# Performance work log

Hardware: AMD Instinct MI355X
Metric: run time of the kernel (lower is better)

Reference implementation:

```python
import jax, jax.numpy as jnp
import numpy as np

USER_NUM = 100000
ITEM_NUM = 50000
D = 64
E = 3200000
B = 16384


def setup_inputs() -> dict:
    key = jax.random.key(0)
    ks = jax.random.split(key, 12)
    user = jax.random.randint(ks[0], (B,), 0, USER_NUM)
    item_i = jax.random.randint(ks[1], (B,), 0, ITEM_NUM)
    item_j = jax.random.randint(ks[2], (B,), 0, ITEM_NUM)
    edge_u = jax.random.randint(ks[3], (E,), 0, USER_NUM)
    edge_i = jax.random.randint(ks[4], (E,), 0, ITEM_NUM)
    edge_val = jax.random.uniform(ks[5], (E,), dtype=jnp.float32)
    # nn.init.normal_(std=0.01)
    user_emb = 0.01 * jax.random.normal(ks[6], (USER_NUM, D), dtype=jnp.float32)
    item_emb = 0.01 * jax.random.normal(ks[7], (ITEM_NUM, D), dtype=jnp.float32)
    old_U_emb = 0.01 * jax.random.normal(ks[8], (USER_NUM, D), dtype=jnp.float32)
    old_I_emb = 0.01 * jax.random.normal(ks[9], (ITEM_NUM, D), dtype=jnp.float32)
    n_U = jax.random.uniform(ks[10], (USER_NUM,), dtype=jnp.float32)
    n_U = n_U / jnp.linalg.norm(n_U)  # pre_self normalizes by L2 norm
    n_I = jax.random.uniform(ks[11], (ITEM_NUM,), dtype=jnp.float32)
    n_I = n_I / jnp.linalg.norm(n_I)
    return {"user": user, "item_i": item_i, "item_j": item_j,
            "edge_u": edge_u, "edge_i": edge_i, "edge_val": edge_val,
            "user_emb": user_emb, "item_emb": item_emb,
            "old_U_emb": old_U_emb, "old_I_emb": old_I_emb,
            "n_U": n_U, "n_I": n_I}


def _spmm(seg_ids, gather_ids, vals, x, num_segments):
    # one hop of sparse adjacency @ dense embeddings: gather -> scale -> scatter-add
    msg = vals[:, None] * x[gather_ids]          # [E, D]
    return jax.ops.segment_sum(msg, seg_ids, num_segments=num_segments)


def reference(user, item_i, item_j, edge_u, edge_i, edge_val,
              user_emb, item_emb, old_U_emb, old_I_emb, n_U, n_I):
    # 3-hop LightGCN-style propagation over bipartite graph
    g1u = _spmm(edge_u, edge_i, edge_val, item_emb, USER_NUM)
    g1i = _spmm(edge_i, edge_u, edge_val, user_emb, ITEM_NUM)
    g2u = _spmm(edge_u, edge_i, edge_val, g1i, USER_NUM)
    g2i = _spmm(edge_i, edge_u, edge_val, g1u, ITEM_NUM)
    g3u = _spmm(edge_u, edge_i, edge_val, g2i, USER_NUM)
    g3i = _spmm(edge_i, edge_u, edge_val, g2u, ITEM_NUM)
    gcn_u = user_emb + 0.5 * g1u + (1.0 / 3.0) * g2u + 0.25 * g3u
    gcn_i = item_emb + 0.5 * g1i + (1.0 / 3.0) * g2i + 0.25 * g3i

    # BPR loss
    u = gcn_u[user]
    ii = gcn_i[item_i]
    ij = gcn_i[item_j]
    pred_i = jnp.sum(u * ii, axis=-1)
    pred_j = jnp.sum(u * ij, axis=-1)
    bpr = -jnp.mean(jax.nn.log_sigmoid(pred_i - pred_j))
    reg = 1e-4 * jnp.mean(jnp.sum(u ** 2 + ii ** 2 + ij ** 2, axis=-1))
    loss_bpr = bpr + reg

    # self-distillation loss (loss_self)
    Ud = jnp.linalg.norm(old_U_emb - gcn_u, axis=1)  # [USER_NUM]
    Id = jnp.linalg.norm(old_I_emb - gcn_i, axis=1)  # [ITEM_NUM]
    loss_self = jnp.dot(Ud, n_U) / USER_NUM + jnp.dot(Id, n_I) / ITEM_NUM

    return jnp.stack([loss_bpr, 100.0 * loss_self,
                      jnp.float32(1.0), jnp.float32(1.0)])
```

## Files before the change

kernel.cpp:

```cpp
#include <hip/hip_runtime.h>

#define USER_NUM 100000
#define ITEM_NUM 50000
#define DD 64
#define NEDGE 3200000
#define NB 16384
#define NSLOT 256

#define ATILE 8192
#define NTILE ((NEDGE + ATILE - 1) / ATILE)
#define USH 9
#define ISH 8
#define UBK ((USER_NUM + (1 << USH) - 1) >> USH)
#define IBK ((ITEM_NUM + (1 << ISH) - 1) >> ISH)
#define NBK (UBK + IBK)
#define CPAD 16
#define HIST_GRID 784

#define FP8_SCALE 64.0f

typedef float v2f __attribute__((ext_vector_type(2)));

__device__ __forceinline__ float waveReduceSum(float x) {
#pragma unroll
    for (int off = 32; off > 0; off >>= 1)
        x += __shfl_down(x, off, 64);
    return x;
}

__device__ __forceinline__ unsigned roundbf(unsigned y) {
    return (y + 0x7fffu + ((y >> 16) & 1u)) >> 16;
}

__device__ __forceinline__ void dec8(const uint2 b, float* f) {
    v2f f0 = __builtin_amdgcn_cvt_pk_f32_fp8(b.x, false);
    v2f f1 = __builtin_amdgcn_cvt_pk_f32_fp8(b.x, true);
    v2f f2 = __builtin_amdgcn_cvt_pk_f32_fp8(b.y, false);
    v2f f3 = __builtin_amdgcn_cvt_pk_f32_fp8(b.y, true);
    f[0] = f0.x; f[1] = f0.y; f[2] = f1.x; f[3] = f1.y;
    f[4] = f2.x; f[5] = f2.y; f[6] = f3.x; f[7] = f3.y;
}
__device__ __forceinline__ void fma8p(const uint2 b, const float v, v2f* a) {
    v2f f0 = __builtin_amdgcn_cvt_pk_f32_fp8(b.x, false);
    v2f f1 = __builtin_amdgcn_cvt_pk_f32_fp8(b.x, true);
    v2f f2 = __builtin_amdgcn_cvt_pk_f32_fp8(b.y, false);
    v2f f3 = __builtin_amdgcn_cvt_pk_f32_fp8(b.y, true);
    const v2f vv = {v, v};
    a[0] += vv * f0;
    a[1] += vv * f1;
    a[2] += vv * f2;
    a[3] += vv * f3;
}
__device__ __forceinline__ uint2 pack_fp8x8(const float* a) {
    int lo = 0, hi = 0;
    lo = __builtin_amdgcn_cvt_pk_fp8_f32(a[0], a[1], lo, false);
    lo = __builtin_amdgcn_cvt_pk_fp8_f32(a[2], a[3], lo, true);
    hi = __builtin_amdgcn_cvt_pk_fp8_f32(a[4], a[5], hi, false);
    hi = __builtin_amdgcn_cvt_pk_fp8_f32(a[6], a[7], hi, true);
    return make_uint2((unsigned)lo, (unsigned)hi);
}

__global__ void __launch_bounds__(256) cvt8_kernel(
    const float4* __restrict__ src, uint2* __restrict__ dst, int n8) {
    int t = blockIdx.x * blockDim.x + threadIdx.x;
    if (t < n8) {
        float4 a = src[2 * t], b = src[2 * t + 1];
        float f[8] = {a.x * FP8_SCALE, a.y * FP8_SCALE, a.z * FP8_SCALE, a.w * FP8_SCALE,
                      b.x * FP8_SCALE, b.y * FP8_SCALE, b.z * FP8_SCALE, b.w * FP8_SCALE};
        dst[t] = pack_fp8x8(f);
    }
}


__global__ void __launch_bounds__(256) coarse_hist(
    const int4* __restrict__ eu4, const int4* __restrict__ ei4,
    int* __restrict__ coarseCnt) {
    __shared__ int lc[NBK];
    const int t = threadIdx.x;
    for (int j = t; j < NBK; j += 256) lc[j] = 0;
    __syncthreads();
    for (int k = blockIdx.x * 256 + t; k < NEDGE / 4; k += HIST_GRID * 256) {
        int4 u = eu4[k];
        int4 i = ei4[k];
        atomicAdd(&lc[u.x >> USH], 1); atomicAdd(&lc[u.y >> USH], 1);
        atomicAdd(&lc[u.z >> USH], 1); atomicAdd(&lc[u.w >> USH], 1);
        atomicAdd(&lc[UBK + (i.x >> ISH)], 1); atomicAdd(&lc[UBK + (i.y >> ISH)], 1);
        atomicAdd(&lc[UBK + (i.z >> ISH)], 1); atomicAdd(&lc[UBK + (i.w >> ISH)], 1);
    }
    __syncthreads();
    for (int j = t; j < NBK; j += 256)
        if (lc[j]) atomicAdd(&coarseCnt[j * CPAD], lc[j]);
}

__global__ void __launch_bounds__(512) coarse_scan(
    const int* __restrict__ cnt, int* __restrict__ base, int* __restrict__ cur) {
    __shared__ int a[512];
    const int t = threadIdx.x;
    int v = (t < UBK) ? cnt[t * CPAD] : 0;
    a[t] = v;
    __syncthreads();
    for (int off = 1; off < 512; off <<= 1) {
        int x = (t >= off) ? a[t - off] : 0;
        __syncthreads();
        a[t] += x;
        __syncthreads();
    }
    if (t < UBK) { base[t] = a[t] - v; cur[t * CPAD] = a[t] - v; }
    __syncthreads();
    v = (t < IBK) ? cnt[(UBK + t) * CPAD] : 0;
    a[t] = v;
    __syncthreads();
    for (int off = 1; off < 512; off <<= 1) {
        int x = (t >= off) ? a[t - off] : 0;
        __syncthreads();
        a[t] += x;
        __syncthreads();
    }
    if (t < IBK) { base[UBK + t] = a[t] - v; cur[(UBK + t) * CPAD] = a[t] - v; }
}

__global__ void __launch_bounds__(256, 2) binA(
    const int* __restrict__ eu, const int* __restrict__ ei,
    const float* __restrict__ ev,
    int* __restrict__ ccur,
    int2* __restrict__ stU, int2* __restrict__ stI) {
    __shared__ int2 pay[ATILE];
    __shared__ unsigned char sbid[ATILE];
    __shared__ int hist[256];
    __shared__ int pscan[256];
    __shared__ int cursor[256];
    __shared__ int delta[256];

    const int t = threadIdx.x;
    const int dirI = blockIdx.y;
    const int tb = blockIdx.x * ATILE;
    const int n = min(ATILE, NEDGE - tb);
    const int* key = dirI ? ei : eu;
    const int SH = dirI ? ISH : USH;

    hist[t] = 0;
    __syncthreads();
    for (int k = t; k < n; k += 256)
        atomicAdd(&hist[key[tb + k] >> SH], 1);
    __syncthreads();
    pscan[t] = hist[t];
    __syncthreads();
    for (int off = 1; off < 256; off <<= 1) {
        int x = (t >= off) ? pscan[t - off] : 0;
        __syncthreads();
        pscan[t] += x;
        __syncthreads();
    }
    {
        const int c = hist[t];
        const int lst = pscan[t] - c;
        cursor[t] = lst;
        int gp = 0;
        if (c > 0) {
            int* gc = dirI ? (ccur + UBK * CPAD) : ccur;
            gp = atomicAdd(&gc[t * CPAD], c);
        }
        delta[t] = gp - lst;
    }
    __syncthreads();
    if (dirI == 0) {
        for (int k = t; k < n; k += 256) {
            const int e = tb + k;
            const int u = eu[e], i = ei[e];
            const int b = u >> USH;
            const int p = atomicAdd(&cursor[b], 1);
            pay[p] = make_int2(((u & ((1 << USH) - 1)) << 16) | i,
                               __float_as_int(ev[e]));
            sbid[p] = (unsigned char)b;
        }
    } else {
        for (int k = t; k < n; k += 256) {
            const int e = tb + k;
            const int u = eu[e], i = ei[e];
            const int b = i >> ISH;
            const int p = atomicAdd(&cursor[b], 1);
            pay[p] = make_int2(((i & ((1 << ISH) - 1)) << 17) | u,
                               __float_as_int(ev[e]));
            sbid[p] = (unsigned char)b;
        }
    }
    __syncthreads();
    int2* st = dirI ? stI : stU;
    for (int p = t; p < n; p += 256)
        st[delta[sbid[p]] + p] = pay[p];
}

__global__ void __launch_bounds__(256) binB(
    const int2* __restrict__ stU, const int2* __restrict__ stI,
    const int* __restrict__ base, const int* __restrict__ cnt,
    int* __restrict__ rpU, int* __restrict__ rpI,
    unsigned* __restrict__ ivU, unsigned* __restrict__ ivI) {
    __shared__ int h[512];
    const int t = threadIdx.x;
    const int b = blockIdx.x;
    if (b < UBK) {
        const int s = base[b], n = cnt[b * CPAD];
        const int dbase = b << USH;
        h[t] = 0; h[t + 256] = 0;
        __syncthreads();
        for (int p = s + t; p < s + n; p += 256)
            atomicAdd(&h[(unsigned)stU[p].x >> 16], 1);
        __syncthreads();
        int o0 = h[t], o1 = h[t + 256];
        for (int off = 1; off < 512; off <<= 1) {
            int x0 = (t >= off) ? h[t - off] : 0;
            int x1 = (t + 256 >= off) ? h[t + 256 - off] : 0;
            __syncthreads();
            h[t] += x0; h[t + 256] += x1;
            __syncthreads();
        }
        int e0 = s + h[t] - o0, e1 = s + h[t + 256] - o1;
        __syncthreads();
        h[t] = e0; h[t + 256] = e1;
        if (dbase + t < USER_NUM) rpU[dbase + t] = e0;
        if (dbase + 256 + t < USER_NUM) rpU[dbase + 256 + t] = e1;
        if (t == 0 && dbase + 512 >= USER_NUM) rpU[USER_NUM] = s + n;
        __syncthreads();
        for (int p = s + t; p < s + n; p += 256) {
            int2 en = stU[p];
            unsigned x = (unsigned)en.x;
            int pos = atomicAdd(&h[x >> 16], 1);
            unsigned bf = roundbf((unsigned)en.y);
            ivU[pos] = (bf << 16) | (x & 0xFFFFu);
        }
    } else {
        const int ib = b - UBK;
        const int s = base[b], n = cnt[b * CPAD];
        const int dbase = ib << ISH;
        h[t] = 0;
        __syncthreads();
        for (int p = s + t; p < s + n; p += 256)
            atomicAdd(&h[(unsigned)stI[p].x >> 17], 1);
        __syncthreads();
        int o0 = h[t];
        for (int off = 1; off < 256; off <<= 1) {
            int x0 = (t >= off) ? h[t - off] : 0;
            __syncthreads();
            h[t] += x0;
            __syncthreads();
        }
        int e0 = s + h[t] - o0;
        __syncthreads();
        h[t] = e0;
        if (dbase + t < ITEM_NUM) rpI[dbase + t] = e0;
        if (t == 0 && dbase + 256 >= ITEM_NUM) rpI[ITEM_NUM] = s + n;
        __syncthreads();
        for (int p = s + t; p < s + n; p += 256) {
            int2 en = stI[p];
            unsigned x = (unsigned)en.x;
            int pos = atomicAdd(&h[x >> 17], 1);
            unsigned v15 = roundbf((unsigned)en.y) & 0x7FFFu;
            ivI[pos] = (v15 << 17) | (x & 0x1FFFFu);
        }
    }
}

#define UW (USER_NUM / 8)
#define IW (ITEM_NUM / 8)

template<bool ISU>
__device__ __forceinline__ void row_accum_own(
    const int* __restrict__ rp, const unsigned* __restrict__ iv,
    const uint2* __restrict__ src, int row, int r, float* acc) {
    const int s = rp[row], e2 = rp[row + 1];
    v2f a0[4] = {{0.f, 0.f}, {0.f, 0.f}, {0.f, 0.f}, {0.f, 0.f}};
    v2f a1[4] = {{0.f, 0.f}, {0.f, 0.f}, {0.f, 0.f}, {0.f, 0.f}};
    int t = s;
    for (; t + 3 < e2; t += 4) {
        const unsigned q0 = iv[t];
        const unsigned q1 = iv[t + 1];
        const unsigned q2 = iv[t + 2];
        const unsigned q3 = iv[t + 3];
        const float v0 = ISU ? __uint_as_float(q0 & 0xFFFF0000u)
                             : __uint_as_float((q0 >> 17) << 16);
        const float v1 = ISU ? __uint_as_float(q1 & 0xFFFF0000u)
                             : __uint_as_float((q1 >> 17) << 16);
        const float v2 = ISU ? __uint_as_float(q2 & 0xFFFF0000u)
                             : __uint_as_float((q2 >> 17) << 16);
        const float v3 = ISU ? __uint_as_float(q3 & 0xFFFF0000u)
                             : __uint_as_float((q3 >> 17) << 16);
        const int x0 = ISU ? (int)(q0 & 0xFFFFu) : (int)(q0 & 0x1FFFFu);
        const int x1 = ISU ? (int)(q1 & 0xFFFFu) : (int)(q1 & 0x1FFFFu);
        const int x2 = ISU ? (int)(q2 & 0xFFFFu) : (int)(q2 & 0x1FFFFu);
        const int x3 = ISU ? (int)(q3 & 0xFFFFu) : (int)(q3 & 0x1FFFFu);
        const uint2 b0 = src[x0 * 8 + r];
        const uint2 b1 = src[x1 * 8 + r];
        const uint2 b2 = src[x2 * 8 + r];
        const uint2 b3 = src[x3 * 8 + r];
        fma8p(b0, v0, a0);
        fma8p(b1, v1, a1);
        fma8p(b2, v2, a0);
        fma8p(b3, v3, a1);
    }
    for (; t < e2; ++t) {
        const unsigned q0 = iv[t];
        const float v0 = ISU ? __uint_as_float(q0 & 0xFFFF0000u)
                             : __uint_as_float((q0 >> 17) << 16);
        const int x0 = ISU ? (int)(q0 & 0xFFFFu) : (int)(q0 & 0x1FFFFu);
        fma8p(src[x0 * 8 + r], v0, a0);
    }
#pragma unroll
    for (int k = 0; k < 4; k++) {
        const v2f sv = a0[k] + a1[k];
        acc[2 * k]     = sv.x;
        acc[2 * k + 1] = sv.y;
    }
}

__global__ void __launch_bounds__(256) gather_hop_f8(
    const int* __restrict__ rpU, const unsigned* __restrict__ ivU,
    const uint2* __restrict__ srcForU, uint2* __restrict__ outU,
    const int* __restrict__ rpI, const unsigned* __restrict__ ivI,
    const uint2* __restrict__ srcForI, uint2* __restrict__ outI) {
    const int lane = threadIdx.x & 63;
    const int sub = lane >> 3;
    const int r = lane & 7;
    const int wave = blockIdx.x * 4 + (threadIdx.x >> 6);
    float acc[8];
    if (wave < UW) {
        const int row = wave * 8 + sub;
        row_accum_own<true>(rpU, ivU, srcForU, row, r, acc);
        outU[row * 8 + r] = pack_fp8x8(acc);
    } else if (wave < UW + IW) {
        const int row = (wave - UW) * 8 + sub;
        row_accum_own<false>(rpI, ivI, srcForI, row, r, acc);
        outI[row * 8 + r] = pack_fp8x8(acc);
    }
}

__global__ void __launch_bounds__(256) gather_hop3(
    const int* __restrict__ rpU, const unsigned* __restrict__ ivU,
    const uint2* __restrict__ srcForU,
    const int* __restrict__ rpI, const unsigned* __restrict__ ivI,
    const uint2* __restrict__ srcForI,
    const float4* __restrict__ embU, const uint2* __restrict__ g1u,
    const uint2* __restrict__ g2u, float4* __restrict__ gcnU,
    const float4* __restrict__ embI, const uint2* __restrict__ g1i,
    const uint2* __restrict__ g2i, float4* __restrict__ gcnI) {
    const int lane = threadIdx.x & 63;
    const int sub = lane >> 3;
    const int r = lane & 7;
    const int wave = blockIdx.x * 4 + (threadIdx.x >> 6);
    float acc[8];
    const float4* emb; const uint2* g1; const uint2* g2; float4* gcn; int row;
    if (wave < UW) {
        row = wave * 8 + sub;
        row_accum_own<true>(rpU, ivU, srcForU, row, r, acc);
        emb = embU; g1 = g1u; g2 = g2u; gcn = gcnU;
    } else if (wave < UW + IW) {
        row = (wave - UW) * 8 + sub;
        row_accum_own<false>(rpI, ivI, srcForI, row, r, acc);
        emb = embI; g1 = g1i; g2 = g2i; gcn = gcnI;
    } else return;
    {
        const float C1 = 0.5f / FP8_SCALE;
        const float C2 = (1.0f / 3.0f) / FP8_SCALE;
        const float C3 = 0.25f / FP8_SCALE;
        float f1[8], f2[8];
        dec8(g1[row * 8 + r], f1);
        dec8(g2[row * 8 + r], f2);
        const float4 e0 = emb[row * 16 + 2 * r];
        const float4 e1 = emb[row * 16 + 2 * r + 1];
        float4 o0, o1;
        o0.x = e0.x + C1 * f1[0] + C2 * f2[0] + C3 * acc[0];
        o0.y = e0.y + C1 * f1[1] + C2 * f2[1] + C3 * acc[1];
        o0.z = e0.z + C1 * f1[2] + C2 * f2[2] + C3 * acc[2];
        o0.w = e0.w + C1 * f1[3] + C2 * f2[3] + C3 * acc[3];
        o1.x = e1.x + C1 * f1[4] + C2 * f2[4] + C3 * acc[4];
        o1.y = e1.y + C1 * f1[5] + C2 * f2[5] + C3 * acc[5];
        o1.z = e1.z + C1 * f1[6] + C2 * f2[6] + C3 * acc[6];
        o1.w = e1.w + C1 * f1[7] + C2 * f2[7] + C3 * acc[7];
        gcn[row * 16 + 2 * r] = o0;
        gcn[row * 16 + 2 * r + 1] = o1;
    }
}

__global__ void __launch_bounds__(256) bpr_loss(
    const int* __restrict__ user, const int* __restrict__ itemI,
    const int* __restrict__ itemJ,
    const float4* __restrict__ gcnU4, const float4* __restrict__ gcnI4,
    float* __restrict__ accs) {
    const int lane = threadIdx.x & 63;
    const int sub = lane >> 4;
    const int r = lane & 15;
    const int W = blockIdx.x * 4 + (threadIdx.x >> 6);
    const int NW = gridDim.x * 4;
    float accB = 0.0f, accR = 0.0f;
    for (int g = W; g < NB / 4; g += NW) {
        const int samp = g * 4 + sub;
        const int uu = user[samp], vi = itemI[samp], vj = itemJ[samp];
        const float4 u  = gcnU4[uu * 16 + r];
        const float4 xi = gcnI4[vi * 16 + r];
        const float4 xj = gcnI4[vj * 16 + r];
        float pi = u.x * xi.x + u.y * xi.y + u.z * xi.z + u.w * xi.w;
        float pj = u.x * xj.x + u.y * xj.y + u.z * xj.z + u.w * xj.w;
        float rg = u.x * u.x + u.y * u.y + u.z * u.z + u.w * u.w
                 + xi.x * xi.x + xi.y * xi.y + xi.z * xi.z + xi.w * xi.w
                 + xj.x * xj.x + xj.y * xj.y + xj.z * xj.z + xj.w * xj.w;
#pragma unroll
        for (int off = 1; off <= 8; off <<= 1) {
            pi += __shfl_xor(pi, off, 64);
            pj += __shfl_xor(pj, off, 64);
            rg += __shfl_xor(rg, off, 64);
        }
        if (r == 0) {
            const float x = pi - pj;
            accB += fmaxf(-x, 0.0f) + log1pf(expf(-fabsf(x)));
            accR += rg;
        }
    }
    accB = waveReduceSum(accB);
    accR = waveReduceSum(accR);
    if (lane == 0) {
        const int slot = W & (NSLOT - 1);
        unsafeAtomicAdd(&accs[0 * NSLOT + slot], accB);
        unsafeAtomicAdd(&accs[1 * NSLOT + slot], accR);
    }
}

__global__ void __launch_bounds__(256) self_loss(
    const float4* __restrict__ oldU4, const float4* __restrict__ oldI4,
    const float4* __restrict__ gcnU4, const float4* __restrict__ gcnI4,
    const float* __restrict__ nU, const float* __restrict__ nI,
    float* __restrict__ accs) {
    const int lane = threadIdx.x & 63;
    const int sub = lane >> 4;
    const int r = lane & 15;
    const int W = blockIdx.x * 4 + (threadIdx.x >> 6);
    const int NW = gridDim.x * 4;
    const int ngroups = (USER_NUM + ITEM_NUM) / 4;
    float accU = 0.0f, accI = 0.0f;
    for (int g = W; g < ngroups; g += NW) {
        const int row = g * 4 + sub;
        const bool isU = row < USER_NUM;
        const int rr = isU ? row : row - USER_NUM;
        const float4 o  = isU ? oldU4[rr * 16 + r] : oldI4[rr * 16 + r];
        const float4 gg = isU ? gcnU4[rr * 16 + r] : gcnI4[rr * 16 + r];
        const float dx = o.x - gg.x, dy = o.y - gg.y;
        const float dz = o.z - gg.z, dw = o.w - gg.w;
        float s = dx * dx + dy * dy + dz * dz + dw * dw;
#pragma unroll
        for (int off = 1; off <= 8; off <<= 1)
            s += __shfl_xor(s, off, 64);
        if (r == 0) {
            const float val = sqrtf(s) * (isU ? nU[rr] : nI[rr]);
            if (isU) accU += val; else accI += val;
        }
    }
    accU = waveReduceSum(accU);
    accI = waveReduceSum(accI);
    if (lane == 0) {
        const int slot = W & (NSLOT - 1);
        unsafeAtomicAdd(&accs[2 * NSLOT + slot], accU);
        unsafeAtomicAdd(&accs[3 * NSLOT + slot], accI);
    }
}

__global__ void __launch_bounds__(64) finalize(const float* __restrict__ accs,
                                               float* __restrict__ out) {
    const int lane = threadIdx.x;
    float s[4];
#pragma unroll
    for (int k = 0; k < 4; k++) {
        float v = 0.0f;
        for (int j = lane; j < NSLOT; j += 64) v += accs[k * NSLOT + j];
        s[k] = waveReduceSum(v);
    }
    if (lane == 0) {
        const float loss_bpr = s[0] / NB + 1e-4f * (s[1] / NB);
        const float loss_self = s[2] / USER_NUM + s[3] / ITEM_NUM;
        out[0] = loss_bpr;
        out[1] = 100.0f * loss_self;
        out[2] = 1.0f;
        out[3] = 1.0f;
    }
}

extern "C" void kernel_launch(void* const* d_in, const int* in_sizes, int n_in,
                              void* d_out, int out_size, void* d_ws, size_t ws_size,
                              hipStream_t stream) {
    const int*   user     = (const int*)d_in[0];
    const int*   item_i   = (const int*)d_in[1];
    const int*   item_j   = (const int*)d_in[2];
    const int*   edge_u   = (const int*)d_in[3];
    const int*   edge_i   = (const int*)d_in[4];
    const float* edge_val = (const float*)d_in[5];
    const float* user_emb = (const float*)d_in[6];
    const float* item_emb = (const float*)d_in[7];
    const float* old_U    = (const float*)d_in[8];
    const float* old_I    = (const float*)d_in[9];
    const float* n_U      = (const float*)d_in[10];
    const float* n_I      = (const float*)d_in[11];
    float* out = (float*)d_out;

    char* base = (char*)d_ws;
    size_t off = 0;
    auto carve = [&](size_t bytes) {
        char* p = base + off;
        off += (bytes + 255) & ~(size_t)255;
        return p;
    };
    int*      coarseCnt = (int*)carve(NBK * CPAD * 4);
    float*    accs      = (float*)carve(4 * NSLOT * 4);
    size_t zero_bytes = off;
    int*      cbase = (int*)carve(NBK * 4);
    int*      ccur  = (int*)carve(NBK * CPAD * 4);
    int*      rpU   = (int*)carve((USER_NUM + 1) * 4);
    int*      rpI   = (int*)carve((ITEM_NUM + 1) * 4);
    unsigned* ivU   = (unsigned*)carve((size_t)NEDGE * 4);
    unsigned* ivI   = (unsigned*)carve((size_t)NEDGE * 4);
    uint2*    ebU8  = (uint2*)carve((size_t)USER_NUM * DD);
    uint2*    ebI8  = (uint2*)carve((size_t)ITEM_NUM * DD);
    uint2*    g1u8  = (uint2*)carve((size_t)USER_NUM * DD);
    uint2*    g1i8  = (uint2*)carve((size_t)ITEM_NUM * DD);
    uint2*    g2u8  = (uint2*)carve((size_t)USER_NUM * DD);
    uint2*    g2i8  = (uint2*)carve((size_t)ITEM_NUM * DD);
    int2*     stU   = (int2*)carve((size_t)NEDGE * 8);
    int2*     stI   = (int2*)carve((size_t)NEDGE * 8);
    float* gcnU = (float*)stU;
    float* gcnI = (float*)stI;

    hipMemsetAsync(d_ws, 0, zero_bytes, stream);

    const dim3 blk(256);

    cvt8_kernel<<<(USER_NUM * 8 + 255) / 256, blk, 0, stream>>>(
        (const float4*)user_emb, ebU8, USER_NUM * 8);
    cvt8_kernel<<<(ITEM_NUM * 8 + 255) / 256, blk, 0, stream>>>(
        (const float4*)item_emb, ebI8, ITEM_NUM * 8);

    coarse_hist<<<HIST_GRID, blk, 0, stream>>>((const int4*)edge_u,
                                               (const int4*)edge_i, coarseCnt);
    coarse_scan<<<1, 512, 0, stream>>>(coarseCnt, cbase, ccur);
    binA<<<dim3(NTILE, 2), blk, 0, stream>>>(edge_u, edge_i, edge_val,
                                             ccur, stU, stI);
    binB<<<NBK, blk, 0, stream>>>(stU, stI, cbase, coarseCnt, rpU, rpI, ivU, ivI);

    const int hop_waves = UW + IW;
    const int hop_grid = (hop_waves + 3) / 4;

    gather_hop_f8<<<hop_grid, blk, 0, stream>>>(rpU, ivU, ebI8, g1u8,
                                                rpI, ivI, ebU8, g1i8);
    gather_hop_f8<<<hop_grid, blk, 0, stream>>>(rpU, ivU, g1i8, g2u8,
                                                rpI, ivI, g1u8, g2i8);
    gather_hop3<<<hop_grid, blk, 0, stream>>>(
        rpU, ivU, g2i8, rpI, ivI, g2u8,
        (const float4*)user_emb, g1u8, g2u8, (float4*)gcnU,
        (const float4*)item_emb, g1i8, g2i8, (float4*)gcnI);

    bpr_loss<<<128, blk, 0, stream>>>(user, item_i, item_j,
                                      (const float4*)gcnU, (const float4*)gcnI, accs);
    self_loss<<<256, blk, 0, stream>>>(
        (const float4*)old_U, (const float4*)old_I,
        (const float4*)gcnU, (const float4*)gcnI, n_U, n_I, accs);
    finalize<<<1, 64, 0, stream>>>(accs, out);
}
```

Before: 593.3 us.

## Fuse self-distillation loss into final hop, deepen gather unroll, shrink binning tile

Folds the self-loss computation into the third gather hop, so the gcn values are used straight from registers. This removes the separate self_loss kernel that re-read gcnU/gcnI and the old embeddings. The per-row gather loop now issues up to 16 index loads and 16 source loads before accumulating, to expose more memory-level parallelism, with 8/4/2/1 tail blocks. The binning tile is halved and binA's launch bounds raised to 4 blocks per CU for more occupancy, at the cost of more tiles and possible register pressure.

```diff
diff --git a/kernel.cpp b/kernel.cpp
--- a/kernel.cpp
+++ b/kernel.cpp
@@ -7,7 +7,7 @@
 #define NB 16384
 #define NSLOT 256
 
-#define ATILE 8192
+#define ATILE 4096
 #define NTILE ((NEDGE + ATILE - 1) / ATILE)
 #define USH 9
 #define ISH 8
@@ -119,7 +119,7 @@
     if (t < IBK) { base[UBK + t] = a[t] - v; cur[(UBK + t) * CPAD] = a[t] - v; }
 }
 
-__global__ void __launch_bounds__(256, 2) binA(
+__global__ void __launch_bounds__(256, 4) binA(
     const int* __restrict__ eu, const int* __restrict__ ei,
     const float* __restrict__ ev,
     int* __restrict__ ccur,
@@ -264,46 +264,43 @@
 #define IW (ITEM_NUM / 8)
 
 template<bool ISU>
+__device__ __forceinline__ int xof(unsigned q) {
+    return ISU ? (int)(q & 0xFFFFu) : (int)(q & 0x1FFFFu);
+}
+template<bool ISU>
+__device__ __forceinline__ float vof(unsigned q) {
+    return ISU ? __uint_as_float(q & 0xFFFF0000u)
+               : __uint_as_float((q >> 17) << 16);
+}
+
+template<bool ISU, int N>
+__device__ __forceinline__ void edge_block(
+    const unsigned* __restrict__ iv, int t,
+    const uint2* __restrict__ srcr, v2f* a0, v2f* a1) {
+    unsigned q[N];
+    uint2 b[N];
+#pragma unroll
+    for (int j = 0; j < N; j++) q[j] = iv[t + j];
+#pragma unroll
+    for (int j = 0; j < N; j++) b[j] = srcr[xof<ISU>(q[j]) * 8];
+#pragma unroll
+    for (int j = 0; j < N; j++) fma8p(b[j], vof<ISU>(q[j]), (j & 1) ? a1 : a0);
+}
+
+template<bool ISU>
 __device__ __forceinline__ void row_accum_own(
     const int* __restrict__ rp, const unsigned* __restrict__ iv,
     const uint2* __restrict__ src, int row, int r, float* acc) {
     const int s = rp[row], e2 = rp[row + 1];
+    const uint2* __restrict__ srcr = src + r;
     v2f a0[4] = {{0.f, 0.f}, {0.f, 0.f}, {0.f, 0.f}, {0.f, 0.f}};
     v2f a1[4] = {{0.f, 0.f}, {0.f, 0.f}, {0.f, 0.f}, {0.f, 0.f}};
     int t = s;
-    for (; t + 3 < e2; t += 4) {
-        const unsigned q0 = iv[t];
-        const unsigned q1 = iv[t + 1];
-        const unsigned q2 = iv[t + 2];
-        const unsigned q3 = iv[t + 3];
-        const float v0 = ISU ? __uint_as_float(q0 & 0xFFFF0000u)
-                             : __uint_as_float((q0 >> 17) << 16);
-        const float v1 = ISU ? __uint_as_float(q1 & 0xFFFF0000u)
-                             : __uint_as_float((q1 >> 17) << 16);
-        const float v2 = ISU ? __uint_as_float(q2 & 0xFFFF0000u)
-                             : __uint_as_float((q2 >> 17) << 16);
-        const float v3 = ISU ? __uint_as_float(q3 & 0xFFFF0000u)
-                             : __uint_as_float((q3 >> 17) << 16);
-        const int x0 = ISU ? (int)(q0 & 0xFFFFu) : (int)(q0 & 0x1FFFFu);
-        const int x1 = ISU ? (int)(q1 & 0xFFFFu) : (int)(q1 & 0x1FFFFu);
-        const int x2 = ISU ? (int)(q2 & 0xFFFFu) : (int)(q2 & 0x1FFFFu);
-        const int x3 = ISU ? (int)(q3 & 0xFFFFu) : (int)(q3 & 0x1FFFFu);
-        const uint2 b0 = src[x0 * 8 + r];
-        const uint2 b1 = src[x1 * 8 + r];
-        const uint2 b2 = src[x2 * 8 + r];
-        const uint2 b3 = src[x3 * 8 + r];
-        fma8p(b0, v0, a0);
-        fma8p(b1, v1, a1);
-        fma8p(b2, v2, a0);
-        fma8p(b3, v3, a1);
-    }
-    for (; t < e2; ++t) {
-        const unsigned q0 = iv[t];
-        const float v0 = ISU ? __uint_as_float(q0 & 0xFFFF0000u)
-                             : __uint_as_float((q0 >> 17) << 16);
-        const int x0 = ISU ? (int)(q0 & 0xFFFFu) : (int)(q0 & 0x1FFFFu);
-        fma8p(src[x0 * 8 + r], v0, a0);
-    }
+    for (; t + 15 < e2; t += 16) edge_block<ISU, 16>(iv, t, srcr, a0, a1);
+    if (t + 7 < e2) { edge_block<ISU, 8>(iv, t, srcr, a0, a1); t += 8; }
+    if (t + 3 < e2) { edge_block<ISU, 4>(iv, t, srcr, a0, a1); t += 4; }
+    if (t + 1 < e2) { edge_block<ISU, 2>(iv, t, srcr, a0, a1); t += 2; }
+    if (t < e2)     edge_block<ISU, 1>(iv, t, srcr, a0, a1);
 #pragma unroll
     for (int k = 0; k < 4; k++) {
         const v2f sv = a0[k] + a1[k];
@@ -341,21 +338,27 @@
     const float4* __restrict__ embU, const uint2* __restrict__ g1u,
     const uint2* __restrict__ g2u, float4* __restrict__ gcnU,
     const float4* __restrict__ embI, const uint2* __restrict__ g1i,
-    const uint2* __restrict__ g2i, float4* __restrict__ gcnI) {
+    const uint2* __restrict__ g2i, float4* __restrict__ gcnI,
+    const float4* __restrict__ oldU4, const float4* __restrict__ oldI4,
+    const float* __restrict__ nU, const float* __restrict__ nI,
+    float* __restrict__ accs) {
     const int lane = threadIdx.x & 63;
     const int sub = lane >> 3;
     const int r = lane & 7;
     const int wave = blockIdx.x * 4 + (threadIdx.x >> 6);
     float acc[8];
     const float4* emb; const uint2* g1; const uint2* g2; float4* gcn; int row;
+    const float4* old4; const float* nrm; bool isU;
     if (wave < UW) {
         row = wave * 8 + sub;
         row_accum_own<true>(rpU, ivU, srcForU, row, r, acc);
         emb = embU; g1 = g1u; g2 = g2u; gcn = gcnU;
+        old4 = oldU4; nrm = nU; isU = true;
     } else if (wave < UW + IW) {
         row = (wave - UW) * 8 + sub;
         row_accum_own<false>(rpI, ivI, srcForI, row, r, acc);
         emb = embI; g1 = g1i; g2 = g2i; gcn = gcnI;
+        old4 = oldI4; nrm = nI; isU = false;
     } else return;
     {
         const float C1 = 0.5f / FP8_SCALE;
@@ -377,6 +380,23 @@
         o1.w = e1.w + C1 * f1[7] + C2 * f2[7] + C3 * acc[7];
         gcn[row * 16 + 2 * r] = o0;
         gcn[row * 16 + 2 * r + 1] = o1;
+        const float4 d0 = old4[row * 16 + 2 * r];
+        const float4 d1 = old4[row * 16 + 2 * r + 1];
+        const float ex = d0.x - o0.x, ey = d0.y - o0.y;
+        const float ez = d0.z - o0.z, ew = d0.w - o0.w;
+        const float fx = d1.x - o1.x, fy = d1.y - o1.y;
+        const float fz = d1.z - o1.z, fw = d1.w - o1.w;
+        float ss = ex * ex + ey * ey + ez * ez + ew * ew
+                 + fx * fx + fy * fy + fz * fz + fw * fw;
+        ss += __shfl_xor(ss, 1, 64);
+        ss += __shfl_xor(ss, 2, 64);
+        ss += __shfl_xor(ss, 4, 64);
+        float val = (r == 0) ? sqrtf(ss) * nrm[row] : 0.0f;
+        val = waveReduceSum(val);
+        if (lane == 0) {
+            const int slot = wave & (NSLOT - 1);
+            unsafeAtomicAdd(&accs[(isU ? 2 : 3) * NSLOT + slot], val);
+        }
     }
 }
 
@@ -420,44 +440,6 @@
         const int slot = W & (NSLOT - 1);
         unsafeAtomicAdd(&accs[0 * NSLOT + slot], accB);
         unsafeAtomicAdd(&accs[1 * NSLOT + slot], accR);
-    }
-}
-
-__global__ void __launch_bounds__(256) self_loss(
-    const float4* __restrict__ oldU4, const float4* __restrict__ oldI4,
-    const float4* __restrict__ gcnU4, const float4* __restrict__ gcnI4,
-    const float* __restrict__ nU, const float* __restrict__ nI,
-    float* __restrict__ accs) {
-    const int lane = threadIdx.x & 63;
-    const int sub = lane >> 4;
-    const int r = lane & 15;
-    const int W = blockIdx.x * 4 + (threadIdx.x >> 6);
-    const int NW = gridDim.x * 4;
-    const int ngroups = (USER_NUM + ITEM_NUM) / 4;
-    float accU = 0.0f, accI = 0.0f;
-    for (int g = W; g < ngroups; g += NW) {
-        const int row = g * 4 + sub;
-        const bool isU = row < USER_NUM;
-        const int rr = isU ? row : row - USER_NUM;
-        const float4 o  = isU ? oldU4[rr * 16 + r] : oldI4[rr * 16 + r];
-        const float4 gg = isU ? gcnU4[rr * 16 + r] : gcnI4[rr * 16 + r];
-        const float dx = o.x - gg.x, dy = o.y - gg.y;
-        const float dz = o.z - gg.z, dw = o.w - gg.w;
-        float s = dx * dx + dy * dy + dz * dz + dw * dw;
-#pragma unroll
-        for (int off = 1; off <= 8; off <<= 1)
-            s += __shfl_xor(s, off, 64);
-        if (r == 0) {
-            const float val = sqrtf(s) * (isU ? nU[rr] : nI[rr]);
-            if (isU) accU += val; else accI += val;
-        }
-    }
-    accU = waveReduceSum(accU);
-    accI = waveReduceSum(accI);
-    if (lane == 0) {
-        const int slot = W & (NSLOT - 1);
-        unsafeAtomicAdd(&accs[2 * NSLOT + slot], accU);
-        unsafeAtomicAdd(&accs[3 * NSLOT + slot], accI);
     }
 }
 
@@ -551,12 +533,10 @@
     gather_hop3<<<hop_grid, blk, 0, stream>>>(
         rpU, ivU, g2i8, rpI, ivI, g2u8,
         (const float4*)user_emb, g1u8, g2u8, (float4*)gcnU,
-        (const float4*)item_emb, g1i8, g2i8, (float4*)gcnI);
+        (const float4*)item_emb, g1i8, g2i8, (float4*)gcnI,
+        (const float4*)old_U, (const float4*)old_I, n_U, n_I, accs);
 
     bpr_loss<<<128, blk, 0, stream>>>(user, item_i, item_j,
                                       (const float4*)gcnU, (const float4*)gcnI, accs);
-    self_loss<<<256, blk, 0, stream>>>(
-        (const float4*)old_U, (const float4*)old_I,
-        (const float4*)gcnU, (const float4*)gcnI, n_U, n_I, accs);
     finalize<<<1, 64, 0, stream>>>(accs, out);
 }
```

Result: faster. 536.3 us (-9.6%).
